# Performance work log

Hardware: AMD Instinct MI355X
Metric: run time of the kernel (lower is better)

## Reference

```python
import jax, jax.numpy as jnp
import numpy as np

N, E, M = 4096, 65536, 16   # nodes, edges, channel multiplicity per degree
MID = 32                    # RadialFunc hidden width (SE3-Transformer default)
EPS = 1e-5                  # BatchNorm1d eps
DEGS = [0, 1]
PAIRS = [(0, 0), (0, 1), (1, 0), (1, 1)]  # (d_in, d_out)


def _bn_relu(x, g, b):
    # BatchNorm1d in training mode (biased batch stats over edges) + ReLU
    mu = x.mean(0, keepdims=True)
    var = ((x - mu) ** 2).mean(0, keepdims=True)
    return jax.nn.relu((x - mu) / jnp.sqrt(var + EPS) * g + b)


def _radial(feat, w1, b1, g1, be1, w2, b2, g2, be2, w3, b3, nf):
    # RadialFunc: Linear-BN-ReLU, Linear-BN-ReLU, Linear -> [E, nc_out, 1, nc_in, 1, nf]
    y = _bn_relu(feat @ w1 + b1, g1, be1)
    y = _bn_relu(y @ w2 + b2, g2, be2)
    y = y @ w3 + b3
    return y.reshape(-1, M, 1, M, 1, nf)


def _forward(h0, h1, r, basis00, basis01, basis10, basis11,
             rw1, rb1, rg1, rbe1, rw2, rb2, rg2, rbe2,
             w3_00, b3_00, w3_01, b3_01, w3_10, b3_10, w3_11, b3_11,
             Wself0, Wself1, edge_src, edge_dst):
    h = {0: h0, 1: h1}
    basis = {(0, 0): basis00, (0, 1): basis01, (1, 0): basis10, (1, 1): basis11}
    w3b3 = {(0, 0): (w3_00, b3_00), (0, 1): (w3_01, b3_01),
            (1, 0): (w3_10, b3_10), (1, 1): (w3_11, b3_11)}
    Wself = {0: Wself0, 1: Wself1}
    # PairwiseConv: per-edge kernel = sum_f R * basis  -> [E, M, 2do+1, M, 2di+1]
    kern = {}
    for p, (di, do) in enumerate(PAIRS):
        nf = 2 * min(di, do) + 1
        w3, b3 = w3b3[(di, do)]
        R = _radial(r, rw1[p], rb1[p], rg1[p], rbe1[p],
                    rw2[p], rb2[p], rg2[p], rbe2[p], w3, b3, nf)
        kern[(di, do)] = (R * basis[(di, do)]).sum(-1)
    cnt = jnp.maximum(
        jax.ops.segment_sum(jnp.ones((E,), h0.dtype), edge_dst, num_segments=N), 1.0)
    outs = []
    for do in DEGS:
        msg = jnp.zeros((E, M, 2 * do + 1), h0.dtype)
        for di in DEGS:
            # per-edge small matmul: kernel @ gathered source feature
            msg = msg + jnp.einsum('eopiq,eiq->eop', kern[(di, do)], h[di][edge_src])
        # self-interaction, flavor='skip': add W @ destination feature per edge
        msg = msg + jnp.einsum('mi,eip->emp', Wself[do][0], h[do][edge_dst])
        s = jax.ops.segment_sum(msg, edge_dst, num_segments=N)  # scatter-mean
        outs.append(s / cnt[:, None, None])
    return tuple(outs)


def setup_inputs() -> dict:
    key = jax.random.key(0)
    ks = jax.random.split(key, 20)
    nrm = lambda k, sh, s=1.0: jax.random.normal(k, sh, jnp.float32) * s
    return {
        'h0': nrm(ks[0], (N, M, 1)),
        'h1': nrm(ks[1], (N, M, 3)),
        'r': jax.random.uniform(ks[2], (E, 1), jnp.float32),
        'basis00': nrm(ks[3], (E, 1, 1, 1, 1, 1)),
        'basis01': nrm(ks[4], (E, 1, 3, 1, 1, 1)),
        'basis10': nrm(ks[5], (E, 1, 1, 1, 3, 1)),
        'basis11': nrm(ks[6], (E, 1, 3, 1, 3, 3)),
        'rw1': nrm(ks[7], (4, 1, MID)),
        'rb1': jnp.zeros((4, MID), jnp.float32),
        'rg1': jnp.ones((4, MID), jnp.float32),
        'rbe1': jnp.zeros((4, MID), jnp.float32),
        'rw2': nrm(ks[8], (4, MID, MID), 1.0 / np.sqrt(MID)),
        'rb2': jnp.zeros((4, MID), jnp.float32),
        'rg2': jnp.ones((4, MID), jnp.float32),
        'rbe2': jnp.zeros((4, MID), jnp.float32),
        'w3_00': nrm(ks[9], (MID, M * M), 1.0 / np.sqrt(MID)),
        'b3_00': jnp.zeros((M * M,), jnp.float32),
        'w3_01': nrm(ks[10], (MID, M * M), 1.0 / np.sqrt(MID)),
        'b3_01': jnp.zeros((M * M,), jnp.float32),
        'w3_10': nrm(ks[11], (MID, M * M), 1.0 / np.sqrt(MID)),
        'b3_10': jnp.zeros((M * M,), jnp.float32),
        'w3_11': nrm(ks[12], (MID, M * M * 3), 1.0 / np.sqrt(MID)),
        'b3_11': jnp.zeros((M * M * 3,), jnp.float32),
        'Wself0': nrm(ks[13], (1, M, M), 1.0 / np.sqrt(M)),
        'Wself1': nrm(ks[14], (1, M, M), 1.0 / np.sqrt(M)),
        'edge_src': jax.random.randint(ks[15], (E,), 0, N),
        'edge_dst': jax.random.randint(ks[16], (E,), 0, N),
    }


def reference(h0, h1, r, basis00, basis01, basis10, basis11,
              rw1, rb1, rg1, rbe1, rw2, rb2, rg2, rbe2,
              w3_00, b3_00, w3_01, b3_01, w3_10, b3_10, w3_11, b3_11,
              Wself0, Wself1, edge_src, edge_dst):
    return _forward(h0, h1, r, basis00, basis01, basis10, basis11,
                    rw1, rb1, rg1, rbe1, rw2, rb2, rg2, rbe2,
                    w3_00, b3_00, w3_01, b3_01, w3_10, b3_10, w3_11, b3_11,
                    Wself0, Wself1, edge_src, edge_dst)
```

## Files before the change

kernel.cpp:

```cpp
#include <hip/hip_runtime.h>

#define N_NODES 4096
#define N_EDGES 65536
#define MID 32
#define BN_EPS 1e-5f

#define WS_RSUM    0
#define WS_RSUMSQ  1
#define WS_ALPHA1  272
#define WS_BETA1   400
#define WS_A2      528
#define WS_S2      656
#define WS_GRAM    5120
#define WS_SUMY    9216
#define WS_W2T     17664
#define WS_MSG_F   262144
#define WS_U00     4456448
#define WS_U01     4521984
#define WS_V10     4587520
#define WS_W11     4784128
#define WS_DEG_I   1024
#define WS_CUR_I   9344
#define WS_OFFS_I  13440
#define WS_ELIST_I 65536
#define WSB_WA     524288
#define WSB_WB     557056
#define WSB_WC     573440

typedef short bf16x8 __attribute__((ext_vector_type(8)));
typedef float f32x4  __attribute__((ext_vector_type(4)));

__device__ __forceinline__ unsigned short f2bf(float x) {
    unsigned u = __float_as_uint(x);
    u += 0x7fffu + ((u >> 16) & 1u);
    return (unsigned short)(u >> 16);
}

__device__ __forceinline__ int wimg_idx(int col, int k) {
    return col * 32 + ((((col >> 1) + (k >> 3)) & 3) << 3) + (k & 7);
}

__global__ void __launch_bounds__(256) k_pre(const float* __restrict__ rw2,
        const float* __restrict__ w300, const float* __restrict__ w301,
        const float* __restrict__ w310, const float* __restrict__ w311,
        const float* __restrict__ bw300, const float* __restrict__ bw301,
        const float* __restrict__ bw310, const float* __restrict__ bw311,
        const float* __restrict__ r, const int* __restrict__ edst,
        const float* __restrict__ h0, const float* __restrict__ h1,
        float* __restrict__ wsf) {
    if (blockIdx.x < 128) {
        int t = blockIdx.x * 256 + threadIdx.x;
        char* wsb = (char*)wsf;
        if (t < 4096) {
            int p = t >> 10, rem = t & 1023, c = rem >> 5, k = rem & 31;
            wsf[WS_W2T + t] = rw2[(p << 10) + (k << 5) + c];
        }
        if (t < 16384) {
            int col = t >> 5, k = t & 31;
            float v = (col < 256) ? w300[(k << 8) + col] : w310[(k << 8) + (col - 256)];
            ((unsigned short*)(wsb + WSB_WA))[wimg_idx(col, k)] = f2bf(v);
        }
        if (t < 8192) {
            int col = t >> 5, k = t & 31;
            ((unsigned short*)(wsb + WSB_WB))[wimg_idx(col, k)] = f2bf(w301[(k << 8) + col]);
        }
        if (t < 24576) {
            int col = t >> 5, k = t & 31;
            int f = col >> 8, rem = col & 255;
            ((unsigned short*)(wsb + WSB_WC))[wimg_idx(col, k)] = f2bf(w311[k * 768 + rem * 3 + f]);
        }
    } else if (blockIdx.x < 384) {
        int e = (blockIdx.x - 128) * 256 + threadIdx.x;
        float v = r[e];
        atomicAdd(((int*)wsf) + WS_DEG_I + edst[e], 1);
        float s = v, ss = v * v;
#pragma unroll
        for (int mk = 32; mk >= 1; mk >>= 1) {
            s  += __shfl_xor(s,  mk, 64);
            ss += __shfl_xor(ss, mk, 64);
        }
        __shared__ float ls[4], lss[4];
        int lane = threadIdx.x & 63, wv = threadIdx.x >> 6;
        if (lane == 0) { ls[wv] = s; lss[wv] = ss; }
        __syncthreads();
        if (threadIdx.x == 0) {
            atomicAdd(wsf + WS_RSUM,   ls[0] + ls[1] + ls[2] + ls[3]);
            atomicAdd(wsf + WS_RSUMSQ, lss[0] + lss[1] + lss[2] + lss[3]);
        }
    } else {
        int g = (blockIdx.x - 384) * 256 + threadIdx.x;
        int n = g >> 4, mo = g & 15;
        float h1r[48];
#pragma unroll
        for (int j = 0; j < 48; ++j) h1r[j] = h1[n * 48 + j];
        float s00 = 0.f, s01 = 0.f;
#pragma unroll
        for (int mi = 0; mi < 16; ++mi) {
            float hv = h0[n * 16 + mi];
            s00 += bw300[mo * 16 + mi] * hv;
            s01 += bw301[mo * 16 + mi] * hv;
        }
        wsf[WS_U00 + n * 16 + mo] = s00;
        wsf[WS_U01 + n * 16 + mo] = s01;
#pragma unroll
        for (int q = 0; q < 3; ++q) {
            float sv = 0.f;
#pragma unroll
            for (int mi = 0; mi < 16; ++mi)
                sv += bw310[mo * 16 + mi] * h1r[mi * 3 + q];
            wsf[WS_V10 + n * 48 + q * 16 + mo] = sv;
        }
#pragma unroll
        for (int f = 0; f < 3; ++f)
#pragma unroll
            for (int q = 0; q < 3; ++q) {
                float sv = 0.f;
#pragma unroll
                for (int mi = 0; mi < 16; ++mi)
                    sv += bw311[(mo * 16 + mi) * 3 + f] * h1r[mi * 3 + q];
                wsf[WS_W11 + n * 144 + (f * 3 + q) * 16 + mo] = sv;
            }
    }
}

__global__ void __launch_bounds__(512) k_gram(const float* __restrict__ r,
        const float* __restrict__ rw1, const float* __restrict__ rg1,
        const float* __restrict__ rbe1, float* __restrict__ wsf) {
    int t = threadIdx.x;
    int wv = t >> 6, lane = t & 63;
    int quad = lane >> 4, lq = lane & 15;
    int p  = __builtin_amdgcn_readfirstlane(wv & 3);
    int mt = __builtin_amdgcn_readfirstlane(wv >> 2);
    float mu_r  = wsf[WS_RSUM] * (1.f / N_EDGES);
    float var_r = wsf[WS_RSUMSQ] * (1.f / N_EDGES) - mu_r * mu_r;
    float al[2], be[2];
#pragma unroll
    for (int hh = 0; hh < 2; ++hh) {
        int ch = p * 32 + hh * 16 + lq;
        float w1 = rw1[ch];
        float a = w1 * rg1[ch] * rsqrtf(w1 * w1 * var_r + BN_EPS);
        al[hh] = a;
        be[hh] = rbe1[ch] - a * mu_r;
    }
    bf16x8 ones;
#pragma unroll
    for (int j = 0; j < 8; ++j) ones[j] = (short)0x3F80;
    f32x4 accG0 = {0.f, 0.f, 0.f, 0.f};
    f32x4 accG1 = {0.f, 0.f, 0.f, 0.f};
    f32x4 accS  = {0.f, 0.f, 0.f, 0.f};
    int ebase = blockIdx.x * 512;
#pragma unroll 1
    for (int ks = 0; ks < 16; ++ks) {
        const float* rp = r + ebase + ks * 32 + quad * 8;
        float4 ra = *(const float4*)(rp);
        float4 rb = *(const float4*)(rp + 4);
        float rv[8] = {ra.x, ra.y, ra.z, ra.w, rb.x, rb.y, rb.z, rb.w};
        bf16x8 fr0, fr1;
#pragma unroll
        for (int j = 0; j < 8; ++j) {
            fr0[j] = (short)f2bf(fmaxf(0.f, al[0] * rv[j] + be[0]));
            fr1[j] = (short)f2bf(fmaxf(0.f, al[1] * rv[j] + be[1]));
        }
        bf16x8 fA = mt ? fr1 : fr0;
        accG0 = __builtin_amdgcn_mfma_f32_16x16x32_bf16(fA, fr0, accG0, 0, 0, 0);
        accG1 = __builtin_amdgcn_mfma_f32_16x16x32_bf16(fA, fr1, accG1, 0, 0, 0);
        accS  = __builtin_amdgcn_mfma_f32_16x16x32_bf16(fA, ones, accS,  0, 0, 0);
    }
    float* G = wsf + WS_GRAM + p * 1024;
#pragma unroll
    for (int reg = 0; reg < 4; ++reg) {
        int k1 = mt * 16 + quad * 4 + reg;
        atomicAdd(&G[k1 * 32 + lq],      accG0[reg]);
        atomicAdd(&G[k1 * 32 + 16 + lq], accG1[reg]);
    }
    if (lq == 0) {
#pragma unroll
        for (int reg = 0; reg < 4; ++reg)
            atomicAdd(wsf + WS_SUMY + p * 32 + mt * 16 + quad * 4 + reg, accS[reg]);
    }
}

__global__ void __launch_bounds__(1024) k_fs(const float* __restrict__ rw1,
        const float* __restrict__ rg1, const float* __restrict__ rbe1,
        const float* __restrict__ rg2, const float* __restrict__ rbe2,
        const float* __restrict__ rb2, float* __restrict__ wsf) {
    int t = threadIdx.x;
    if (t < 128) {
        float mu_r  = wsf[WS_RSUM] * (1.f / N_EDGES);
        float var_r = wsf[WS_RSUMSQ] * (1.f / N_EDGES) - mu_r * mu_r;
        float w1 = rw1[t];
        float al = w1 * rg1[t] * rsqrtf(w1 * w1 * var_r + BN_EPS);
        wsf[WS_ALPHA1 + t] = al;
        wsf[WS_BETA1  + t] = rbe1[t] - al * mu_r;
        int p = t >> 5, c = t & 31;
        const float* G = wsf + WS_GRAM + p * 1024;
        const float* w = wsf + WS_W2T + p * 1024 + c * 32;
        float invE = 1.f / N_EDGES;
        float s1 = 0.f;
#pragma unroll 1
        for (int k = 0; k < 32; ++k) s1 += w[k] * (wsf[WS_SUMY + p * 32 + k] * invE);
        float q = 0.f;
#pragma unroll 1
        for (int k1 = 0; k1 < 32; ++k1) {
            float a = 0.f;
#pragma unroll
            for (int k2 = 0; k2 < 32; ++k2) a += w[k2] * G[k1 * 32 + k2];
            q += w[k1] * a;
        }
        float var = q * invE - s1 * s1;
        float a2 = rg2[t] * rsqrtf(var + BN_EPS);
        wsf[WS_A2 + t] = a2;
        float mu2 = rb2[t] + s1;
        wsf[WS_S2 + t] = rbe2[t] - mu2 * a2;
    }
    __shared__ int sdata[1024];
    const int* deg = ((const int*)wsf) + WS_DEG_I;
    int* offs = ((int*)wsf) + WS_OFFS_I;
    int* cur  = ((int*)wsf) + WS_CUR_I;
    int v0 = deg[t * 4], v1 = deg[t * 4 + 1], v2 = deg[t * 4 + 2], v3 = deg[t * 4 + 3];
    sdata[t] = v0 + v1 + v2 + v3;
    __syncthreads();
    for (int off = 1; off < 1024; off <<= 1) {
        int x = sdata[t];
        int y = (t >= off) ? sdata[t - off] : 0;
        __syncthreads();
        sdata[t] = x + y;
        __syncthreads();
    }
    int excl = (t == 0) ? 0 : sdata[t - 1];
    int o0 = excl, o1 = excl + v0, o2 = o1 + v1, o3 = o2 + v2;
    offs[t * 4] = o0;     cur[t * 4] = o0;
    offs[t * 4 + 1] = o1; cur[t * 4 + 1] = o1;
    offs[t * 4 + 2] = o2; cur[t * 4 + 2] = o2;
    offs[t * 4 + 3] = o3; cur[t * 4 + 3] = o3;
    if (t == 1023) offs[4096] = sdata[1023];
}

__global__ void __launch_bounds__(256) k_cb(const int* __restrict__ edst,
        const float* __restrict__ b00, const float* __restrict__ b01,
        const float* __restrict__ b10, const float* __restrict__ b11,
        const int* __restrict__ esrc, float* __restrict__ wsf,
        float* __restrict__ msg) {
    if (blockIdx.x < 256) {
        int e = blockIdx.x * 256 + threadIdx.x;
        int d = edst[e];
        int* cur   = ((int*)wsf) + WS_CUR_I;
        int* elist = ((int*)wsf) + WS_ELIST_I;
        int pos = atomicAdd(&cur[d], 1);
        elist[pos] = e;
        return;
    }
    int g = (blockIdx.x - 256) * 256 + threadIdx.x;
    int e = g >> 2, quad = g & 3;
    int s = esrc[e];
    float4 u00q = *(const float4*)(wsf + WS_U00 + s * 16 + quad * 4);
    float b00v = b00[e];
    float m0[4];
#pragma unroll
    for (int rr = 0; rr < 4; ++rr) m0[rr] = b00v * ((const float*)&u00q)[rr];
#pragma unroll
    for (int q = 0; q < 3; ++q) {
        float4 vq = *(const float4*)(wsf + WS_V10 + s * 48 + q * 16 + quad * 4);
        float bq = b10[e * 3 + q];
#pragma unroll
        for (int rr = 0; rr < 4; ++rr) m0[rr] += bq * ((const float*)&vq)[rr];
    }
    {
        float4 w = {m0[0], m0[1], m0[2], m0[3]};
        *(float4*)(msg + (size_t)e * 64 + quad * 4) = w;
    }
    float4 u01q = *(const float4*)(wsf + WS_U01 + s * 16 + quad * 4);
    float bo0 = b01[e * 3 + 0], bo1 = b01[e * 3 + 1], bo2 = b01[e * 3 + 2];
    float m1[4][3];
#pragma unroll
    for (int rr = 0; rr < 4; ++rr) {
        float u = ((const float*)&u01q)[rr];
        m1[rr][0] = bo0 * u; m1[rr][1] = bo1 * u; m1[rr][2] = bo2 * u;
    }
#pragma unroll
    for (int f = 0; f < 3; ++f)
#pragma unroll
        for (int q = 0; q < 3; ++q) {
            float4 wq = *(const float4*)(wsf + WS_W11 + s * 144 + (f * 3 + q) * 16 + quad * 4);
#pragma unroll
            for (int o = 0; o < 3; ++o) {
                float bas = b11[e * 27 + o * 9 + q * 3 + f];
#pragma unroll
                for (int rr = 0; rr < 4; ++rr) m1[rr][o] += bas * ((const float*)&wq)[rr];
            }
        }
    float* base = msg + (size_t)e * 64 + 16 + quad * 12;
    float4 w0 = {m1[0][0], m1[0][1], m1[0][2], m1[1][0]};
    float4 w1 = {m1[1][1], m1[1][2], m1[2][0], m1[2][1]};
    float4 w2 = {m1[2][2], m1[3][0], m1[3][1], m1[3][2]};
    *(float4*)(base)     = w0;
    *(float4*)(base + 4) = w1;
    *(float4*)(base + 8) = w2;
}

__device__ __forceinline__ void y2_lds16(int p, int el, int c0, float rv,
                                         const float* __restrict__ wsf,
                                         const float* __restrict__ rb2, char* dst) {
    float y1[MID];
#pragma unroll
    for (int k = 0; k < MID; ++k)
        y1[k] = fmaxf(0.f, wsf[WS_ALPHA1 + p * 32 + k] * rv + wsf[WS_BETA1 + p * 32 + k]);
    unsigned short h[16];
#pragma unroll
    for (int cc = 0; cc < 16; ++cc) {
        int c = c0 + cc;
        float x = rb2[p * 32 + c];
#pragma unroll
        for (int k = 0; k < MID; ++k) x += y1[k] * wsf[WS_W2T + p * 1024 + c * 32 + k];
        h[cc] = f2bf(fmaxf(0.f, wsf[WS_A2 + p * 32 + c] * x + wsf[WS_S2 + p * 32 + c]));
    }
#pragma unroll
    for (int q = 0; q < 2; ++q) {
        int4 pk;
        pk.x = (int)h[q * 8 + 0] | ((int)h[q * 8 + 1] << 16);
        pk.y = (int)h[q * 8 + 2] | ((int)h[q * 8 + 3] << 16);
        pk.z = (int)h[q * 8 + 4] | ((int)h[q * 8 + 5] << 16);
        pk.w = (int)h[q * 8 + 6] | ((int)h[q * 8 + 7] << 16);
        int jc = (c0 >> 3) + q;
        int slot = ((el >> 1) + jc) & 3;
        *(int4*)(dst + el * 64 + slot * 16) = pk;
    }
}

__global__ void __launch_bounds__(512, 2) k_msg(const float* __restrict__ r,
        const float* __restrict__ h0, const float* __restrict__ h1,
        const float* __restrict__ b00, const float* __restrict__ b01,
        const float* __restrict__ b10, const float* __restrict__ b11,
        const float* __restrict__ rb2,
        const int* __restrict__ esrc,
        const float* __restrict__ wsf, float* __restrict__ msg) {
    extern __shared__ char smem[];
    short* w3s = (short*)smem;
    const char* wsb = (const char*)wsf;
    int t = threadIdx.x;
    int wv = t >> 6, lane = t & 63;
    int quad = lane >> 4, lq = lane & 15;
    int eb = blockIdx.x << 8;
    int woff = (((lq >> 1) + quad) & 3) << 3;
    int yoff = (((lq >> 1) + quad) & 3) << 4;

    {
        const float4* src = (const float4*)(wsb + WSB_WA);
        float4* dst = (float4*)smem;
#pragma unroll
        for (int i = 0; i < 4; ++i) dst[i * 512 + t] = src[i * 512 + t];
    }
    {
        int p = __builtin_amdgcn_readfirstlane((t >> 8) * 2);
        int el = t & 255;
        float rv = r[eb + el];
        char* dst = smem + 32768 + (t >> 8) * 16384;
        y2_lds16(p, el, 0, rv, wsf, rb2, dst);
        y2_lds16(p, el, 16, rv, wsf, rb2, dst);
    }
    __syncthreads();
#pragma unroll
    for (int g2 = 0; g2 < 2; ++g2) {
        int el = (wv * 2 + g2) * 16 + lq;
        int e = eb + el;
        int s = esrc[e];
        bf16x8 bf0 = *(const bf16x8*)(smem + 32768 + el * 64 + yoff);
        bf16x8 bf2 = *(const bf16x8*)(smem + 49152 + el * 64 + yoff);
        float4 h0q = *(const float4*)(h0 + s * 16 + quad * 4);
        float4 hv0 = *(const float4*)(h1 + s * 48 + quad * 12);
        float4 hv1 = *(const float4*)(h1 + s * 48 + quad * 12 + 4);
        float4 hv2 = *(const float4*)(h1 + s * 48 + quad * 12 + 8);
        float b00v = b00[e];
        float bq0 = b10[e * 3 + 0], bq1 = b10[e * 3 + 1], bq2 = b10[e * 3 + 2];
        float gq0 = bq0 * hv0.x + bq1 * hv0.y + bq2 * hv0.z;
        float gq1 = bq0 * hv0.w + bq1 * hv1.x + bq2 * hv1.y;
        float gq2 = bq0 * hv1.z + bq1 * hv1.w + bq2 * hv2.x;
        float gq3 = bq0 * hv2.y + bq1 * hv2.z + bq2 * hv2.w;
        float4 a0v = *(const float4*)(msg + (size_t)e * 64 + quad * 4);
        float a0[4] = {a0v.x, a0v.y, a0v.z, a0v.w};
#pragma unroll
        for (int m = 0; m < 16; ++m) {
            bf16x8 af = *(const bf16x8*)(w3s + (m * 16 + lq) * 32 + woff);
            f32x4 dd = __builtin_amdgcn_mfma_f32_16x16x32_bf16(af, bf0, (f32x4){0.f,0.f,0.f,0.f}, 0, 0, 0);
            float partial = dd[0] * h0q.x + dd[1] * h0q.y + dd[2] * h0q.z + dd[3] * h0q.w;
            partial += __shfl_xor(partial, 16);
            partial += __shfl_xor(partial, 32);
            a0[m & 3] += (quad == (m >> 2)) ? b00v * partial : 0.f;
        }
#pragma unroll
        for (int m = 0; m < 16; ++m) {
            bf16x8 af = *(const bf16x8*)(w3s + (256 + m * 16 + lq) * 32 + woff);
            f32x4 dd = __builtin_amdgcn_mfma_f32_16x16x32_bf16(af, bf2, (f32x4){0.f,0.f,0.f,0.f}, 0, 0, 0);
            float partial = dd[0] * gq0 + dd[1] * gq1 + dd[2] * gq2 + dd[3] * gq3;
            partial += __shfl_xor(partial, 16);
            partial += __shfl_xor(partial, 32);
            a0[m & 3] += (quad == (m >> 2)) ? partial : 0.f;
        }
        float4 w = {a0[0], a0[1], a0[2], a0[3]};
        *(float4*)(msg + (size_t)e * 64 + quad * 4) = w;
    }
    __syncthreads();

    {
        const float4* src = (const float4*)(wsb + WSB_WB);
        float4* dst = (float4*)smem;
#pragma unroll
        for (int i = 0; i < 2; ++i) dst[i * 512 + t] = src[i * 512 + t];
    }
    {
        int el = t & 255, c0 = (t >> 8) * 16;
        y2_lds16(1, el, c0, r[eb + el], wsf, rb2, smem + 16384);
    }
    __syncthreads();
#pragma unroll
    for (int g2 = 0; g2 < 2; ++g2) {
        int el = (wv * 2 + g2) * 16 + lq;
        int e = eb + el;
        int s = esrc[e];
        bf16x8 bf1 = *(const bf16x8*)(smem + 16384 + el * 64 + yoff);
        float4 h0q = *(const float4*)(h0 + s * 16 + quad * 4);
        float d1[4] = {0.f, 0.f, 0.f, 0.f};
#pragma unroll
        for (int m = 0; m < 16; ++m) {
            bf16x8 af = *(const bf16x8*)(w3s + (m * 16 + lq) * 32 + woff);
            f32x4 dd = __builtin_amdgcn_mfma_f32_16x16x32_bf16(af, bf1, (f32x4){0.f,0.f,0.f,0.f}, 0, 0, 0);
            float partial = dd[0] * h0q.x + dd[1] * h0q.y + dd[2] * h0q.z + dd[3] * h0q.w;
            partial += __shfl_xor(partial, 16);
            partial += __shfl_xor(partial, 32);
            d1[m & 3] += (quad == (m >> 2)) ? partial : 0.f;
        }
        float bo0 = b01[e * 3 + 0], bo1 = b01[e * 3 + 1], bo2 = b01[e * 3 + 2];
        float* base = msg + (size_t)e * 64 + 16 + quad * 12;
        float4 r0 = *(const float4*)(base);
        float4 r1 = *(const float4*)(base + 4);
        float4 r2 = *(const float4*)(base + 8);
        float4 w0 = {r0.x + bo0 * d1[0], r0.y + bo1 * d1[0], r0.z + bo2 * d1[0], r0.w + bo0 * d1[1]};
        float4 w1 = {r1.x + bo1 * d1[1], r1.y + bo2 * d1[1], r1.z + bo0 * d1[2], r1.w + bo1 * d1[2]};
        float4 w2 = {r2.x + bo2 * d1[2], r2.y + bo0 * d1[3], r2.z + bo1 * d1[3], r2.w + bo2 * d1[3]};
        *(float4*)(base)     = w0;
        *(float4*)(base + 4) = w1;
        *(float4*)(base + 8) = w2;
    }
    __syncthreads();

    {
        const float4* src = (const float4*)(wsb + WSB_WC);
        float4* dst = (float4*)smem;
#pragma unroll
        for (int i = 0; i < 6; ++i) dst[i * 512 + t] = src[i * 512 + t];
    }
    {
        int el = t & 255, c0 = (t >> 8) * 16;
        y2_lds16(3, el, c0, r[eb + el], wsf, rb2, smem + 49152);
    }
    __syncthreads();
#pragma unroll
    for (int g2 = 0; g2 < 2; ++g2) {
        int el = (wv * 2 + g2) * 16 + lq;
        int e = eb + el;
        int s = esrc[e];
        bf16x8 bf3 = *(const bf16x8*)(smem + 49152 + el * 64 + yoff);
        float4 hv0 = *(const float4*)(h1 + s * 48 + quad * 12);
        float4 hv1 = *(const float4*)(h1 + s * 48 + quad * 12 + 4);
        float4 hv2 = *(const float4*)(h1 + s * 48 + quad * 12 + 8);
        float h1v[4][3] = {{hv0.x, hv0.y, hv0.z}, {hv0.w, hv1.x, hv1.y},
                           {hv1.z, hv1.w, hv2.x}, {hv2.y, hv2.z, hv2.w}};
        float m1[4][3];
#pragma unroll
        for (int rr = 0; rr < 4; ++rr)
#pragma unroll
            for (int o = 0; o < 3; ++o) m1[rr][o] = 0.f;
#pragma unroll
        for (int f = 0; f < 3; ++f) {
            float Tf[4][3];
#pragma unroll
            for (int o = 0; o < 3; ++o) {
                float bv0 = b11[e * 27 + o * 9 + 0 + f];
                float bv1 = b11[e * 27 + o * 9 + 3 + f];
                float bv2 = b11[e * 27 + o * 9 + 6 + f];
#pragma unroll
                for (int rr = 0; rr < 4; ++rr)
                    Tf[rr][o] = h1v[rr][0] * bv0 + h1v[rr][1] * bv1 + h1v[rr][2] * bv2;
            }
#pragma unroll
            for (int m = 0; m < 16; ++m) {
                int colb = f * 256 + m * 16 + lq;
                bf16x8 af = *(const bf16x8*)(w3s + colb * 32 + woff);
                f32x4 dd = __builtin_amdgcn_mfma_f32_16x16x32_bf16(af, bf3, (f32x4){0.f,0.f,0.f,0.f}, 0, 0, 0);
#pragma unroll
                for (int o = 0; o < 3; ++o) {
                    float po = dd[0] * Tf[0][o] + dd[1] * Tf[1][o] + dd[2] * Tf[2][o] + dd[3] * Tf[3][o];
                    po += __shfl_xor(po, 16);
                    po += __shfl_xor(po, 32);
                    m1[m & 3][o] += (quad == (m >> 2)) ? po : 0.f;
                }
            }
        }
        float* base = msg + (size_t)e * 64 + 16 + quad * 12;
        float4 r0 = *(const float4*)(base);
        float4 r1 = *(const float4*)(base + 4);
        float4 r2 = *(const float4*)(base + 8);
        float4 w0 = {m1[0][0] + r0.x, m1[0][1] + r0.y, m1[0][2] + r0.z, m1[1][0] + r0.w};
        float4 w1 = {m1[1][1] + r1.x, m1[1][2] + r1.y, m1[2][0] + r1.z, m1[2][1] + r1.w};
        float4 w2 = {m1[2][2] + r2.x, m1[3][0] + r2.y, m1[3][1] + r2.z, m1[3][2] + r2.w};
        *(float4*)(base)     = w0;
        *(float4*)(base + 4) = w1;
        *(float4*)(base + 8) = w2;
    }
}

__global__ void __launch_bounds__(256) k_gather(const float* __restrict__ h0,
        const float* __restrict__ h1, const float* __restrict__ Wself0,
        const float* __restrict__ Wself1, const float* __restrict__ wsf,
        float* __restrict__ out) {
    int wv = threadIdx.x >> 6, lane = threadIdx.x & 63;
    int n = blockIdx.x * 4 + wv;
    const int* offs  = ((const int*)wsf) + WS_OFFS_I;
    const int* elist = ((const int*)wsf) + WS_ELIST_I;
    const float* msg = wsf + WS_MSG_F;
    int start = offs[n], end = offs[n + 1];
    int deg = end - start;
    float acc = 0.f;
    for (int j0 = 0; j0 < deg; j0 += 64) {
        int cnt = min(64, deg - j0);
        int eidv = (j0 + lane < deg) ? elist[start + j0 + lane] : 0;
        int jj = 0;
        for (; jj + 3 < cnt; jj += 4) {
            int e0 = __shfl(eidv, jj), e1 = __shfl(eidv, jj + 1);
            int e2 = __shfl(eidv, jj + 2), e3 = __shfl(eidv, jj + 3);
            float v0 = msg[(size_t)e0 * 64 + lane];
            float v1 = msg[(size_t)e1 * 64 + lane];
            float v2 = msg[(size_t)e2 * 64 + lane];
            float v3 = msg[(size_t)e3 * 64 + lane];
            acc += (v0 + v1) + (v2 + v3);
        }
        for (; jj < cnt; ++jj) {
            int eid = __shfl(eidv, jj);
            acc += msg[(size_t)eid * 64 + lane];
        }
    }
    float self = 0.f;
    if (lane < 16) {
        int m = lane;
#pragma unroll
        for (int i = 0; i < 16; ++i) self += Wself0[m * 16 + i] * h0[n * 16 + i];
    } else {
        int idx = lane - 16; int m = idx / 3, o = idx % 3;
#pragma unroll
        for (int i = 0; i < 16; ++i) self += Wself1[m * 16 + i] * h1[n * 48 + i * 3 + o];
    }
    float c = (float)(deg > 0 ? deg : 1);
    float res = acc / c + (deg > 0 ? self : 0.f);
    if (lane < 16) out[n * 16 + lane] = res;
    else           out[65536 + n * 48 + (lane - 16)] = res;
}

extern "C" void kernel_launch(void* const* d_in, const int* in_sizes, int n_in,
                              void* d_out, int out_size, void* d_ws, size_t ws_size,
                              hipStream_t stream) {
    const float* h0   = (const float*)d_in[0];
    const float* h1   = (const float*)d_in[1];
    const float* r    = (const float*)d_in[2];
    const float* b00  = (const float*)d_in[3];
    const float* b01  = (const float*)d_in[4];
    const float* b10  = (const float*)d_in[5];
    const float* b11  = (const float*)d_in[6];
    const float* rw1  = (const float*)d_in[7];
    const float* rg1  = (const float*)d_in[9];
    const float* rbe1 = (const float*)d_in[10];
    const float* rw2  = (const float*)d_in[11];
    const float* rb2  = (const float*)d_in[12];
    const float* rg2  = (const float*)d_in[13];
    const float* rbe2 = (const float*)d_in[14];
    const float* w300 = (const float*)d_in[15];
    const float* bw300= (const float*)d_in[16];
    const float* w301 = (const float*)d_in[17];
    const float* bw301= (const float*)d_in[18];
    const float* w310 = (const float*)d_in[19];
    const float* bw310= (const float*)d_in[20];
    const float* w311 = (const float*)d_in[21];
    const float* bw311= (const float*)d_in[22];
    const float* Wself0 = (const float*)d_in[23];
    const float* Wself1 = (const float*)d_in[24];
    const int* esrc = (const int*)d_in[25];
    const int* edst = (const int*)d_in[26];
    float* out = (float*)d_out;
    float* wsf = (float*)d_ws;
    float* msg = wsf + WS_MSG_F;

    static bool attr_set = false;
    if (!attr_set) {
        hipFuncSetAttribute((const void*)k_msg,
                            hipFuncAttributeMaxDynamicSharedMemorySize, 65536);
        attr_set = true;
    }

    hipMemsetAsync(d_ws, 0, 37376, stream);

    k_pre<<<640, 256, 0, stream>>>(rw2, w300, w301, w310, w311,
                                   bw300, bw301, bw310, bw311, r, edst, h0, h1, wsf);
    k_gram<<<128, 512, 0, stream>>>(r, rw1, rg1, rbe1, wsf);
    k_fs<<<1, 1024, 0, stream>>>(rw1, rg1, rbe1, rg2, rbe2, rb2, wsf);
    k_cb<<<1280, 256, 0, stream>>>(edst, b00, b01, b10, b11, esrc, wsf, msg);
    k_msg<<<256, 512, 65536, stream>>>(r, h0, h1, b00, b01, b10, b11, rb2,
                                       esrc, wsf, msg);
    k_gather<<<1024, 256, 0, stream>>>(h0, h1, Wself0, Wself1, wsf, out);
}
```

Before: 249.9 us.

## Precompute piecewise-linear second radial layer and fold k_cb terms into k_msg

The first radial layer is a ReLU of an affine function of the scalar r, so the second layer's pre-activation is piecewise linear in r with at most 32 breakpoints. k_fs now sorts the breakpoints and tabulates slope and intercept per segment, and k_msg replaces the 32x32 matvec per edge with a segment count and one FMA per channel. The low-rank message terms (U00, V10, U01, W11) that k_cb used to compute and write to msg are now computed inside k_msg. This removes the msg read-modify-write passes and k_cb's work, leaving a lighter bucket-only kernel. The cost is a serial selection sort in a single block and more register pressure in k_msg.

```diff
diff --git a/kernel.cpp b/kernel.cpp
--- a/kernel.cpp
+++ b/kernel.cpp
@@ -11,9 +11,11 @@
 #define WS_BETA1   400
 #define WS_A2      528
 #define WS_S2      656
+#define WS_BP      784
 #define WS_GRAM    5120
 #define WS_SUMY    9216
 #define WS_W2T     17664
+#define WS_PWL     24576
 #define WS_MSG_F   262144
 #define WS_U00     4456448
 #define WS_U01     4521984
@@ -214,6 +216,7 @@
         wsf[WS_S2 + t] = rbe2[t] - mu2 * a2;
     }
     __shared__ int sdata[1024];
+    __shared__ float sbp[128];
     const int* deg = ((const int*)wsf) + WS_DEG_I;
     int* offs = ((int*)wsf) + WS_OFFS_I;
     int* cur  = ((int*)wsf) + WS_CUR_I;
@@ -234,86 +237,74 @@
     offs[t * 4 + 2] = o2; cur[t * 4 + 2] = o2;
     offs[t * 4 + 3] = o3; cur[t * 4 + 3] = o3;
     if (t == 1023) offs[4096] = sdata[1023];
-}
-
-__global__ void __launch_bounds__(256) k_cb(const int* __restrict__ edst,
-        const float* __restrict__ b00, const float* __restrict__ b01,
-        const float* __restrict__ b10, const float* __restrict__ b11,
-        const int* __restrict__ esrc, float* __restrict__ wsf,
-        float* __restrict__ msg) {
-    if (blockIdx.x < 256) {
-        int e = blockIdx.x * 256 + threadIdx.x;
-        int d = edst[e];
-        int* cur   = ((int*)wsf) + WS_CUR_I;
-        int* elist = ((int*)wsf) + WS_ELIST_I;
-        int pos = atomicAdd(&cur[d], 1);
-        elist[pos] = e;
-        return;
-    }
-    int g = (blockIdx.x - 256) * 256 + threadIdx.x;
-    int e = g >> 2, quad = g & 3;
-    int s = esrc[e];
-    float4 u00q = *(const float4*)(wsf + WS_U00 + s * 16 + quad * 4);
-    float b00v = b00[e];
-    float m0[4];
-#pragma unroll
-    for (int rr = 0; rr < 4; ++rr) m0[rr] = b00v * ((const float*)&u00q)[rr];
-#pragma unroll
-    for (int q = 0; q < 3; ++q) {
-        float4 vq = *(const float4*)(wsf + WS_V10 + s * 48 + q * 16 + quad * 4);
-        float bq = b10[e * 3 + q];
-#pragma unroll
-        for (int rr = 0; rr < 4; ++rr) m0[rr] += bq * ((const float*)&vq)[rr];
-    }
-    {
-        float4 w = {m0[0], m0[1], m0[2], m0[3]};
-        *(float4*)(msg + (size_t)e * 64 + quad * 4) = w;
-    }
-    float4 u01q = *(const float4*)(wsf + WS_U01 + s * 16 + quad * 4);
-    float bo0 = b01[e * 3 + 0], bo1 = b01[e * 3 + 1], bo2 = b01[e * 3 + 2];
-    float m1[4][3];
-#pragma unroll
-    for (int rr = 0; rr < 4; ++rr) {
-        float u = ((const float*)&u01q)[rr];
-        m1[rr][0] = bo0 * u; m1[rr][1] = bo1 * u; m1[rr][2] = bo2 * u;
-    }
-#pragma unroll
-    for (int f = 0; f < 3; ++f)
-#pragma unroll
-        for (int q = 0; q < 3; ++q) {
-            float4 wq = *(const float4*)(wsf + WS_W11 + s * 144 + (f * 3 + q) * 16 + quad * 4);
-#pragma unroll
-            for (int o = 0; o < 3; ++o) {
-                float bas = b11[e * 27 + o * 9 + q * 3 + f];
-#pragma unroll
-                for (int rr = 0; rr < 4; ++rr) m1[rr][o] += bas * ((const float*)&wq)[rr];
+
+    if (t < 128) {
+        float alk = wsf[WS_ALPHA1 + t], bek = wsf[WS_BETA1 + t];
+        float bp = (alk != 0.f) ? (-bek / alk) : 3.0e38f;
+        sbp[t] = bp;
+        wsf[WS_BP + t] = bp;
+    }
+    __syncthreads();
+    if (t < 128) {
+        int p = t >> 5, c = t & 31;
+        const float* alp = wsf + WS_ALPHA1 + p * 32;
+        const float* bep = wsf + WS_BETA1 + p * 32;
+        const float* wrow = wsf + WS_W2T + p * 1024 + c * 32;
+        float a2 = wsf[WS_A2 + p * 32 + c], s2v = wsf[WS_S2 + p * 32 + c];
+        float A = 0.f, B = rb2[p * 32 + c];
+#pragma unroll 1
+        for (int k = 0; k < 32; ++k) {
+            float ak = alp[k], bk = bep[k], wk = wrow[k];
+            if (ak < 0.f)       { A += ak * wk; B += bk * wk; }
+            else if (ak == 0.f && bk > 0.f) { B += bk * wk; }
+        }
+        float* outp = wsf + WS_PWL + p * 2112 + c;
+        outp[0]  = a2 * A;
+        outp[32] = a2 * B + s2v;
+        unsigned used = 0;
+#pragma unroll 1
+        for (int j = 1; j <= 32; ++j) {
+            int kmin = 0; float bmin = 3.5e38f;
+#pragma unroll 1
+            for (int k = 0; k < 32; ++k) {
+                float b = sbp[p * 32 + k];
+                bool ok = !((used >> k) & 1) && (b < bmin);
+                kmin = ok ? k : kmin;
+                bmin = ok ? b : bmin;
             }
-        }
-    float* base = msg + (size_t)e * 64 + 16 + quad * 12;
-    float4 w0 = {m1[0][0], m1[0][1], m1[0][2], m1[1][0]};
-    float4 w1 = {m1[1][1], m1[1][2], m1[2][0], m1[2][1]};
-    float4 w2 = {m1[2][2], m1[3][0], m1[3][1], m1[3][2]};
-    *(float4*)(base)     = w0;
-    *(float4*)(base + 4) = w1;
-    *(float4*)(base + 8) = w2;
-}
-
-__device__ __forceinline__ void y2_lds16(int p, int el, int c0, float rv,
-                                         const float* __restrict__ wsf,
-                                         const float* __restrict__ rb2, char* dst) {
-    float y1[MID];
-#pragma unroll
-    for (int k = 0; k < MID; ++k)
-        y1[k] = fmaxf(0.f, wsf[WS_ALPHA1 + p * 32 + k] * rv + wsf[WS_BETA1 + p * 32 + k]);
+            used |= (1u << kmin);
+            float ak = alp[kmin], bk = bep[kmin], wk = wrow[kmin];
+            if (ak > 0.f)      { A += ak * wk; B += bk * wk; }
+            else if (ak < 0.f) { A -= ak * wk; B -= bk * wk; }
+            outp[j * 64]      = a2 * A;
+            outp[j * 64 + 32] = a2 * B + s2v;
+        }
+    }
+}
+
+__global__ void __launch_bounds__(256) k_bucket(const int* __restrict__ edst,
+                                                float* __restrict__ wsf) {
+    int e = blockIdx.x * 256 + threadIdx.x;
+    int d = edst[e];
+    int* cur   = ((int*)wsf) + WS_CUR_I;
+    int* elist = ((int*)wsf) + WS_ELIST_I;
+    int pos = atomicAdd(&cur[d], 1);
+    elist[pos] = e;
+}
+
+__device__ __forceinline__ void y2_pwl16(int p, int el, int c0, float rv,
+                                         const float* __restrict__ wsf, char* dst) {
+    int j = 0;
+#pragma unroll
+    for (int k4 = 0; k4 < 8; ++k4) {
+        float4 bp = *(const float4*)(wsf + WS_BP + p * 32 + k4 * 4);
+        j += (rv > bp.x) + (rv > bp.y) + (rv > bp.z) + (rv > bp.w);
+    }
+    const float* ta = wsf + WS_PWL + p * 2112 + j * 64 + c0;
     unsigned short h[16];
 #pragma unroll
-    for (int cc = 0; cc < 16; ++cc) {
-        int c = c0 + cc;
-        float x = rb2[p * 32 + c];
-#pragma unroll
-        for (int k = 0; k < MID; ++k) x += y1[k] * wsf[WS_W2T + p * 1024 + c * 32 + k];
-        h[cc] = f2bf(fmaxf(0.f, wsf[WS_A2 + p * 32 + c] * x + wsf[WS_S2 + p * 32 + c]));
-    }
+    for (int cc = 0; cc < 16; ++cc)
+        h[cc] = f2bf(fmaxf(0.f, ta[cc] * rv + ta[32 + cc]));
 #pragma unroll
     for (int q = 0; q < 2; ++q) {
         int4 pk;
@@ -331,7 +322,6 @@
         const float* __restrict__ h0, const float* __restrict__ h1,
         const float* __restrict__ b00, const float* __restrict__ b01,
         const float* __restrict__ b10, const float* __restrict__ b11,
-        const float* __restrict__ rb2,
         const int* __restrict__ esrc,
         const float* __restrict__ wsf, float* __restrict__ msg) {
     extern __shared__ char smem[];
@@ -343,6 +333,7 @@
     int eb = blockIdx.x << 8;
     int woff = (((lq >> 1) + quad) & 3) << 3;
     int yoff = (((lq >> 1) + quad) & 3) << 4;
+    float d1c[2][4];
 
     {
         const float4* src = (const float4*)(wsb + WSB_WA);
@@ -355,8 +346,8 @@
         int el = t & 255;
         float rv = r[eb + el];
         char* dst = smem + 32768 + (t >> 8) * 16384;
-        y2_lds16(p, el, 0, rv, wsf, rb2, dst);
-        y2_lds16(p, el, 16, rv, wsf, rb2, dst);
+        y2_pwl16(p, el, 0, rv, wsf, dst);
+        y2_pwl16(p, el, 16, rv, wsf, dst);
     }
     __syncthreads();
 #pragma unroll
@@ -376,8 +367,17 @@
         float gq1 = bq0 * hv0.w + bq1 * hv1.x + bq2 * hv1.y;
         float gq2 = bq0 * hv1.z + bq1 * hv1.w + bq2 * hv2.x;
         float gq3 = bq0 * hv2.y + bq1 * hv2.z + bq2 * hv2.w;
-        float4 a0v = *(const float4*)(msg + (size_t)e * 64 + quad * 4);
-        float a0[4] = {a0v.x, a0v.y, a0v.z, a0v.w};
+        float4 u00q = *(const float4*)(wsf + WS_U00 + s * 16 + quad * 4);
+        float a0[4];
+#pragma unroll
+        for (int rr = 0; rr < 4; ++rr) a0[rr] = b00v * ((const float*)&u00q)[rr];
+#pragma unroll
+        for (int q = 0; q < 3; ++q) {
+            float4 vq = *(const float4*)(wsf + WS_V10 + s * 48 + q * 16 + quad * 4);
+            float bq = (q == 0) ? bq0 : (q == 1) ? bq1 : bq2;
+#pragma unroll
+            for (int rr = 0; rr < 4; ++rr) a0[rr] += bq * ((const float*)&vq)[rr];
+        }
 #pragma unroll
         for (int m = 0; m < 16; ++m) {
             bf16x8 af = *(const bf16x8*)(w3s + (m * 16 + lq) * 32 + woff);
@@ -409,7 +409,7 @@
     }
     {
         int el = t & 255, c0 = (t >> 8) * 16;
-        y2_lds16(1, el, c0, r[eb + el], wsf, rb2, smem + 16384);
+        y2_pwl16(1, el, c0, r[eb + el], wsf, smem + 16384);
     }
     __syncthreads();
 #pragma unroll
@@ -429,17 +429,8 @@
             partial += __shfl_xor(partial, 32);
             d1[m & 3] += (quad == (m >> 2)) ? partial : 0.f;
         }
-        float bo0 = b01[e * 3 + 0], bo1 = b01[e * 3 + 1], bo2 = b01[e * 3 + 2];
-        float* base = msg + (size_t)e * 64 + 16 + quad * 12;
-        float4 r0 = *(const float4*)(base);
-        float4 r1 = *(const float4*)(base + 4);
-        float4 r2 = *(const float4*)(base + 8);
-        float4 w0 = {r0.x + bo0 * d1[0], r0.y + bo1 * d1[0], r0.z + bo2 * d1[0], r0.w + bo0 * d1[1]};
-        float4 w1 = {r1.x + bo1 * d1[1], r1.y + bo2 * d1[1], r1.z + bo0 * d1[2], r1.w + bo1 * d1[2]};
-        float4 w2 = {r2.x + bo2 * d1[2], r2.y + bo0 * d1[3], r2.z + bo1 * d1[3], r2.w + bo2 * d1[3]};
-        *(float4*)(base)     = w0;
-        *(float4*)(base + 4) = w1;
-        *(float4*)(base + 8) = w2;
+#pragma unroll
+        for (int rr = 0; rr < 4; ++rr) d1c[g2][rr] = d1[rr];
     }
     __syncthreads();
 
@@ -451,7 +442,7 @@
     }
     {
         int el = t & 255, c0 = (t >> 8) * 16;
-        y2_lds16(3, el, c0, r[eb + el], wsf, rb2, smem + 49152);
+        y2_pwl16(3, el, c0, r[eb + el], wsf, smem + 49152);
     }
     __syncthreads();
 #pragma unroll
@@ -465,11 +456,26 @@
         float4 hv2 = *(const float4*)(h1 + s * 48 + quad * 12 + 8);
         float h1v[4][3] = {{hv0.x, hv0.y, hv0.z}, {hv0.w, hv1.x, hv1.y},
                            {hv1.z, hv1.w, hv2.x}, {hv2.y, hv2.z, hv2.w}};
+        float bo0 = b01[e * 3 + 0], bo1 = b01[e * 3 + 1], bo2 = b01[e * 3 + 2];
+        float4 u01q = *(const float4*)(wsf + WS_U01 + s * 16 + quad * 4);
         float m1[4][3];
 #pragma unroll
-        for (int rr = 0; rr < 4; ++rr)
-#pragma unroll
-            for (int o = 0; o < 3; ++o) m1[rr][o] = 0.f;
+        for (int rr = 0; rr < 4; ++rr) {
+            float u = d1c[g2][rr] + ((const float*)&u01q)[rr];
+            m1[rr][0] = bo0 * u; m1[rr][1] = bo1 * u; m1[rr][2] = bo2 * u;
+        }
+#pragma unroll
+        for (int f = 0; f < 3; ++f)
+#pragma unroll
+            for (int q = 0; q < 3; ++q) {
+                float4 wq = *(const float4*)(wsf + WS_W11 + s * 144 + (f * 3 + q) * 16 + quad * 4);
+#pragma unroll
+                for (int o = 0; o < 3; ++o) {
+                    float bas = b11[e * 27 + o * 9 + q * 3 + f];
+#pragma unroll
+                    for (int rr = 0; rr < 4; ++rr) m1[rr][o] += bas * ((const float*)&wq)[rr];
+                }
+            }
 #pragma unroll
         for (int f = 0; f < 3; ++f) {
             float Tf[4][3];
@@ -497,12 +503,9 @@
             }
         }
         float* base = msg + (size_t)e * 64 + 16 + quad * 12;
-        float4 r0 = *(const float4*)(base);
-        float4 r1 = *(const float4*)(base + 4);
-        float4 r2 = *(const float4*)(base + 8);
-        float4 w0 = {m1[0][0] + r0.x, m1[0][1] + r0.y, m1[0][2] + r0.z, m1[1][0] + r0.w};
-        float4 w1 = {m1[1][1] + r1.x, m1[1][2] + r1.y, m1[2][0] + r1.z, m1[2][1] + r1.w};
-        float4 w2 = {m1[2][2] + r2.x, m1[3][0] + r2.y, m1[3][1] + r2.z, m1[3][2] + r2.w};
+        float4 w0 = {m1[0][0], m1[0][1], m1[0][2], m1[1][0]};
+        float4 w1 = {m1[1][1], m1[1][2], m1[2][0], m1[2][1]};
+        float4 w2 = {m1[2][2], m1[3][0], m1[3][1], m1[3][2]};
         *(float4*)(base)     = w0;
         *(float4*)(base + 4) = w1;
         *(float4*)(base + 8) = w2;
@@ -601,8 +604,8 @@
                                    bw300, bw301, bw310, bw311, r, edst, h0, h1, wsf);
     k_gram<<<128, 512, 0, stream>>>(r, rw1, rg1, rbe1, wsf);
     k_fs<<<1, 1024, 0, stream>>>(rw1, rg1, rbe1, rg2, rbe2, rb2, wsf);
-    k_cb<<<1280, 256, 0, stream>>>(edst, b00, b01, b10, b11, esrc, wsf, msg);
-    k_msg<<<256, 512, 65536, stream>>>(r, h0, h1, b00, b01, b10, b11, rb2,
+    k_bucket<<<256, 256, 0, stream>>>(edst, wsf);
+    k_msg<<<256, 512, 65536, stream>>>(r, h0, h1, b00, b01, b10, b11,
                                        esrc, wsf, msg);
     k_gather<<<1024, 256, 0, stream>>>(h0, h1, Wself0, Wself1, wsf, out);
 }
```

Measured after the change: 300.6 us. 20.3% more time.
